# Kernel optimization log

Hardware: AMD Instinct MI355X
Metric: run time of the kernel (lower is better)

The kernel has to match this reference:

```python
import jax, jax.numpy as jnp
import numpy as np

N = 50000   # nodes
K = 8       # fixed in-degree per node (edges sorted by target)
NQ = 400000 # quadruplets
TWO_PI = 2.0 * np.pi


def setup_inputs() -> dict:
    key = jax.random.key(0)
    k1, k2 = jax.random.split(key)
    pos = jax.random.normal(k1, (N, 3), dtype=jnp.float32) * 3.0
    # ring-structured graph: node i receives edges from (i+1..i+K) mod N.
    # Edges sorted by target i with exactly K per node -> edges into node n
    # occupy slots [n*K, n*K+K). Since N > 2K, a node is never its own
    # 2-hop self (idx_i != idx_k always holds, matching torch's mask).
    i = np.repeat(np.arange(N, dtype=np.int32), K)
    d = np.tile(np.arange(1, K + 1, dtype=np.int32), N)
    j = (i + d) % N
    edge_index = jnp.asarray(np.stack([j, i]), dtype=jnp.int32)  # [2, E]
    q_index = jax.random.randint(k2, (4, NQ), 0, N, dtype=jnp.int32)
    return {"pos": pos, "edge_index": edge_index, "q_index": q_index}


def _geometry(pos, edge_index, q_index):
    j, i = edge_index[0], edge_index[1]
    E = j.shape[0]

    rel = pos[i] - pos[j]
    dist = jnp.sqrt(jnp.sum(rel * rel, axis=-1))                 # [E]

    # ---- triplets: for edge e=(j->i), k ranges over in-neighbors of j ----
    ar = jnp.arange(K, dtype=j.dtype)
    idx_kj = (j[:, None] * K + ar[None, :]).reshape(-1)          # [T] edge ids k->j
    idx_ji = jnp.repeat(jnp.arange(E, dtype=j.dtype), K)         # [T] edge ids j->i
    idx_i = i[idx_ji]
    idx_j = j[idx_ji]
    idx_k = j[idx_kj]

    pos_ji = pos[idx_i] - pos[idx_j]                             # [T,3]
    pos_jk = pos[idx_k] - pos[idx_j]                             # [T,3]
    a = jnp.sum(pos_ji * pos_jk, axis=-1)
    b = jnp.linalg.norm(jnp.cross(pos_ji, pos_jk), axis=-1)
    angle = jnp.arctan2(b, a)                                    # [T]

    # ---- quadruplets: k_n ranges over the K in-neighbors of idx_j ----
    kn_edges = idx_j[:, None] * K + ar[None, :]                  # [T,K]
    idx_k_n = j[kn_edges]                                        # [T,K]
    pos_jkn = pos[idx_k_n] - pos[idx_j][:, None, :]              # [T,K,3]
    plane1 = jnp.cross(pos_ji, pos_jk)                           # [T,3]
    plane2 = jnp.cross(pos_ji[:, None, :], pos_jkn)              # [T,K,3]
    dist_ji = jnp.sqrt(jnp.sum(pos_ji * pos_ji, axis=-1))        # [T]
    a2 = jnp.sum(plane1[:, None, :] * plane2, axis=-1)           # [T,K]
    b2 = jnp.sum(jnp.cross(plane1[:, None, :], plane2) * pos_ji[:, None, :], axis=-1) / dist_ji[:, None]
    torsion = jnp.arctan2(b2, a2)
    torsion = jnp.where(torsion <= 0, torsion + TWO_PI, torsion)
    valid = (idx_k_n != idx_i[:, None]) & (idx_k_n != idx_k[:, None])
    # scatter_min over quadruplets grouped by triplet == masked row-min
    torsiona = jnp.min(jnp.where(valid, torsion, jnp.inf), axis=-1)  # [T]

    plane_s = 0.5 * jnp.sin(angle) * dist[idx_kj] * dist[idx_ji]     # [T]

    # ---- tetrahedron volumes for quadruplets q_index [4,NQ] ----
    pq = pos[q_index.T]                                          # [NQ,4,3]
    v1 = pq[:, 1] - pq[:, 0]
    v2 = pq[:, 2] - pq[:, 0]
    v3 = pq[:, 3] - pq[:, 0]
    volume = jnp.abs(jnp.sum(jnp.cross(v1, v2) * v3, axis=-1)) / 6.0  # [NQ]

    return dist, angle, torsiona, plane_s, volume, idx_ji, idx_kj


def reference(pos, edge_index, q_index):
    dist, angle, torsiona, plane_s, volume, idx_ji, idx_kj = _geometry(pos, edge_index, q_index)
    # matches torch return: (dist, angle, torsiona, torsiona, torsiona, plane_s, volume, idx_ji, idx_kj)
    return (dist, angle, torsiona, torsiona, torsiona, plane_s, volume, idx_ji, idx_kj)
```

## Files before the change

kernel.cpp:

```cpp
#include <hip/hip_runtime.h>

#define KDEG 8
constexpr float TWO_PI_F = 6.28318530717958647692f;
constexpr float PI_F = 3.14159265358979323846f;
constexpr float PI_2_F = 1.57079632679489661923f;
constexpr float BIG_F = 1000.0f;

struct F3 { float x, y, z; };
__device__ __forceinline__ F3 f3sub(F3 a, F3 b) { return {a.x - b.x, a.y - b.y, a.z - b.z}; }
__device__ __forceinline__ float f3dot(F3 a, F3 b) { return a.x * b.x + a.y * b.y + a.z * b.z; }
__device__ __forceinline__ F3 f3cross(F3 a, F3 b) {
  return {a.y * b.z - a.z * b.y, a.z * b.x - a.x * b.z, a.x * b.y - a.y * b.x};
}
__device__ __forceinline__ F3 ldpos(const float* __restrict__ p, int idx) {
  return {p[3 * idx], p[3 * idx + 1], p[3 * idx + 2]};
}

__device__ __forceinline__ float fast_atan01(float z) {
  float z2 = z * z;
  return z * fmaf(z2, -0.19194795f, 0.97239411f);
}

__device__ __forceinline__ float fast_atan2(float y, float x) {
  float ax = fabsf(x), ay = fabsf(y);
  float mx = fmaxf(ax, ay);
  float mn = fminf(ax, ay);
  float z = mn * __builtin_amdgcn_rcpf(fmaxf(mx, 1e-30f));
  float r = fast_atan01(z);
  r = (ay > ax) ? (PI_2_F - r) : r;
  r = (x < 0.0f) ? (PI_F - r) : r;
  return (y < 0.0f) ? -r : r;
}

__device__ __forceinline__ float fast_atan2_pos(float y, float x) {
  float ax = fabsf(x);
  float mx = fmaxf(ax, y);
  float mn = fminf(ax, y);
  float z = mn * __builtin_amdgcn_rcpf(fmaxf(mx, 1e-30f));
  float r = fast_atan01(z);
  r = (y > ax) ? (PI_2_F - r) : r;
  return (x < 0.0f) ? (PI_F - r) : r;
}

__device__ __forceinline__ void st4(float* p, float a, float b, float c, float d) {
  float4 v = {a, b, c, d};
  *reinterpret_cast<float4*>(p) = v;
}

__device__ __forceinline__ void edge_work(
    int e,
    const float* __restrict__ pos,
    const int* __restrict__ ei_j,
    const int* __restrict__ ei_i,
    float* __restrict__ out,
    int off_angle, int off_t0, int off_t1, int off_t2,
    int off_ps, int off_iji, int off_ikj)
{
  int j = ei_j[e];
  int i = ei_i[e];
  (void)i;

  int base = j * KDEG;
  int nbr[KDEG];
#pragma unroll
  for (int n = 0; n < KDEG; n++) nbr[n] = ei_j[base + n];

  F3 pj = ldpos(pos, j);
  F3 pi = ldpos(pos, i);
  F3 pji = f3sub(pi, pj);
  float d2 = f3dot(pji, pji);
  float inv_dji = rsqrtf(d2);
  float dji = d2 * inv_dji;
  out[e] = dji;

  const F3 G = {0.53452248f, -0.26726124f, 0.80178373f};
  F3 e1 = f3cross(pji, G);
  F3 e2 = f3cross(pji, e1);
  float L2 = f3dot(e1, e1);
  float invL = rsqrtf(fmaxf(L2, 1e-30f));
  float djinvL = dji * invL;

  float phi[KDEG], phiw[KDEG], ang[KDEG], hb[KDEG];
#pragma unroll
  for (int n = 0; n < KDEG; n++) {
    F3 u = f3sub(ldpos(pos, nbr[n]), pj);
    float s = f3dot(pji, u);
    float a = f3dot(e1, u);
    float b = f3dot(e2, u) * inv_dji;
    phi[n] = fast_atan2(b, a);
    phiw[n] = phi[n] + TWO_PI_F;
    float perp = sqrtf(fmaf(a, a, b * b));
    float bfull = perp * djinvL;
    ang[n] = fast_atan2_pos(bfull, s);
    hb[n] = 0.5f * bfull;
  }

  int t0 = e * KDEG;
  st4(out + off_angle + t0,     ang[0], ang[1], ang[2], ang[3]);
  st4(out + off_angle + t0 + 4, ang[4], ang[5], ang[6], ang[7]);
  st4(out + off_ps + t0,        hb[0], hb[1], hb[2], hb[3]);
  st4(out + off_ps + t0 + 4,    hb[4], hb[5], hb[6], hb[7]);
  float fe = (float)e;
  st4(out + off_iji + t0,     fe, fe, fe, fe);
  st4(out + off_iji + t0 + 4, fe, fe, fe, fe);
  float fb = (float)base;
  st4(out + off_ikj + t0,     fb, fb + 1.0f, fb + 2.0f, fb + 3.0f);
  st4(out + off_ikj + t0 + 4, fb + 4.0f, fb + 5.0f, fb + 6.0f, fb + 7.0f);

  float succ[KDEG];
#pragma unroll
  for (int n = 0; n < KDEG; n++) succ[n] = BIG_F;
#pragma unroll
  for (int kk = 0; kk < KDEG; kk++) {
#pragma unroll
    for (int n = kk + 1; n < KDEG; n++) {
      bool gt = phi[n] > phi[kk];
      float ckk = gt ? phi[n] : phiw[n];
      float cn  = gt ? phiw[kk] : phi[kk];
      succ[kk] = fminf(succ[kk], ckk);
      succ[n]  = fminf(succ[n], cn);
    }
  }
  float mn[KDEG];
#pragma unroll
  for (int n = 0; n < KDEG; n++) mn[n] = succ[n] - phi[n];

  st4(out + off_t0 + t0,     mn[0], mn[1], mn[2], mn[3]);
  st4(out + off_t0 + t0 + 4, mn[4], mn[5], mn[6], mn[7]);
  st4(out + off_t1 + t0,     mn[0], mn[1], mn[2], mn[3]);
  st4(out + off_t1 + t0 + 4, mn[4], mn[5], mn[6], mn[7]);
  st4(out + off_t2 + t0,     mn[0], mn[1], mn[2], mn[3]);
  st4(out + off_t2 + t0 + 4, mn[4], mn[5], mn[6], mn[7]);
}

__device__ __forceinline__ void volume_work(
    int t,
    const float* __restrict__ pos,
    const int* __restrict__ q,
    float* __restrict__ out,
    int NQ, int off_vol)
{
  int q0 = q[t];
  int q1 = q[t + NQ];
  int q2 = q[t + 2 * NQ];
  int q3 = q[t + 3 * NQ];
  F3 p0 = ldpos(pos, q0);
  F3 p1 = ldpos(pos, q1);
  F3 p2 = ldpos(pos, q2);
  F3 p3 = ldpos(pos, q3);
  F3 v1 = f3sub(p1, p0);
  F3 v2 = f3sub(p2, p0);
  F3 v3 = f3sub(p3, p0);
  float vol = fabsf(f3dot(f3cross(v1, v2), v3)) * (1.0f / 6.0f);
  out[off_vol + t] = vol;
}

__global__ __launch_bounds__(256) void fused_kernel(
    const float* __restrict__ pos,
    const int* __restrict__ ei_j,
    const int* __restrict__ ei_i,
    const int* __restrict__ q,
    float* __restrict__ out,
    int E, int NQ, int nbE,
    int off_angle, int off_t0, int off_t1, int off_t2,
    int off_ps, int off_vol, int off_iji, int off_ikj)
{
  int b = blockIdx.x;
  if (b < nbE) {
    int e = b * blockDim.x + threadIdx.x;
    if (e < E)
      edge_work(e, pos, ei_j, ei_i, out,
                off_angle, off_t0, off_t1, off_t2, off_ps, off_iji, off_ikj);
  } else {
    int t = (b - nbE) * blockDim.x + threadIdx.x;
    if (t < NQ)
      volume_work(t, pos, q, out, NQ, off_vol);
  }
}

extern "C" void kernel_launch(void* const* d_in, const int* in_sizes, int n_in,
                              void* d_out, int out_size, void* d_ws, size_t ws_size,
                              hipStream_t stream) {
  const float* pos = (const float*)d_in[0];
  const int* edge_index = (const int*)d_in[1];
  const int* q_index = (const int*)d_in[2];

  const int E = in_sizes[1] / 2;
  const int NQ = in_sizes[2] / 4;
  const int T = E * KDEG;

  const int* ei_j = edge_index;
  const int* ei_i = edge_index + E;

  float* out = (float*)d_out;

  const int off_angle = E;
  const int off_t0 = off_angle + T;
  const int off_t1 = off_t0 + T;
  const int off_t2 = off_t1 + T;
  const int off_ps = off_t2 + T;
  const int off_vol = off_ps + T;
  const int off_iji = off_vol + NQ;
  const int off_ikj = off_iji + T;
  (void)out_size; (void)d_ws; (void)ws_size; (void)n_in;

  const int blk = 256;
  const int nbE = (E + blk - 1) / blk;
  const int nbQ = (NQ + blk - 1) / blk;

  fused_kernel<<<nbE + nbQ, blk, 0, stream>>>(
      pos, ei_j, ei_i, q_index, out, E, NQ, nbE,
      off_angle, off_t0, off_t1, off_t2, off_ps, off_vol, off_iji, off_ikj);
}
```

Measured before the change: 31.49 us.

## Map one thread per triplet and compute torsion min via lane shuffles

Replaces the one-thread-per-edge mapping, where each thread handled all 8 triplets, with one thread per triplet. The eight threads of an edge exchange their phi values through __shfl_xor to find the angular successor. This raises parallelism eightfold, lowers per-thread register pressure and gives coalesced scalar stores in place of per-thread float4 stores. In exchange, the edge-level loads and the basis setup are repeated in every triplet thread, and the total thread count grows.

```diff
diff --git a/kernel.cpp b/kernel.cpp
--- a/kernel.cpp
+++ b/kernel.cpp
@@ -42,13 +42,8 @@
   return (x < 0.0f) ? (PI_F - r) : r;
 }
 
-__device__ __forceinline__ void st4(float* p, float a, float b, float c, float d) {
-  float4 v = {a, b, c, d};
-  *reinterpret_cast<float4*>(p) = v;
-}
-
-__device__ __forceinline__ void edge_work(
-    int e,
+__device__ __forceinline__ void tri_work(
+    int t,
     const float* __restrict__ pos,
     const int* __restrict__ ei_j,
     const int* __restrict__ ei_i,
@@ -56,22 +51,18 @@
     int off_angle, int off_t0, int off_t1, int off_t2,
     int off_ps, int off_iji, int off_ikj)
 {
+  int e = t >> 3;
+  int kk = t & 7;
+
   int j = ei_j[e];
   int i = ei_i[e];
-  (void)i;
-
-  int base = j * KDEG;
-  int nbr[KDEG];
-#pragma unroll
-  for (int n = 0; n < KDEG; n++) nbr[n] = ei_j[base + n];
-
   F3 pj = ldpos(pos, j);
   F3 pi = ldpos(pos, i);
   F3 pji = f3sub(pi, pj);
   float d2 = f3dot(pji, pji);
   float inv_dji = rsqrtf(d2);
   float dji = d2 * inv_dji;
-  out[e] = dji;
+  if (kk == 0) out[e] = dji;
 
   const F3 G = {0.53452248f, -0.26726124f, 0.80178373f};
   F3 e1 = f3cross(pji, G);
@@ -80,57 +71,33 @@
   float invL = rsqrtf(fmaxf(L2, 1e-30f));
   float djinvL = dji * invL;
 
-  float phi[KDEG], phiw[KDEG], ang[KDEG], hb[KDEG];
+  int k = ei_j[j * KDEG + kk];
+  F3 u = f3sub(ldpos(pos, k), pj);
+  float s = f3dot(pji, u);
+  float a = f3dot(e1, u);
+  float b = f3dot(e2, u) * inv_dji;
+  float phi = fast_atan2(b, a);
+  float perp = sqrtf(fmaf(a, a, b * b));
+  float bfull = perp * djinvL;
+  float ang = fast_atan2_pos(bfull, s);
+  float hb = 0.5f * bfull;
+
+  float succ = BIG_F;
 #pragma unroll
-  for (int n = 0; n < KDEG; n++) {
-    F3 u = f3sub(ldpos(pos, nbr[n]), pj);
-    float s = f3dot(pji, u);
-    float a = f3dot(e1, u);
-    float b = f3dot(e2, u) * inv_dji;
-    phi[n] = fast_atan2(b, a);
-    phiw[n] = phi[n] + TWO_PI_F;
-    float perp = sqrtf(fmaf(a, a, b * b));
-    float bfull = perp * djinvL;
-    ang[n] = fast_atan2_pos(bfull, s);
-    hb[n] = 0.5f * bfull;
+  for (int m = 1; m < KDEG; m++) {
+    float php = __shfl_xor(phi, m, KDEG);
+    float cand = (php > phi) ? php : php + TWO_PI_F;
+    succ = fminf(succ, cand);
   }
+  float tors = succ - phi;
 
-  int t0 = e * KDEG;
-  st4(out + off_angle + t0,     ang[0], ang[1], ang[2], ang[3]);
-  st4(out + off_angle + t0 + 4, ang[4], ang[5], ang[6], ang[7]);
-  st4(out + off_ps + t0,        hb[0], hb[1], hb[2], hb[3]);
-  st4(out + off_ps + t0 + 4,    hb[4], hb[5], hb[6], hb[7]);
-  float fe = (float)e;
-  st4(out + off_iji + t0,     fe, fe, fe, fe);
-  st4(out + off_iji + t0 + 4, fe, fe, fe, fe);
-  float fb = (float)base;
-  st4(out + off_ikj + t0,     fb, fb + 1.0f, fb + 2.0f, fb + 3.0f);
-  st4(out + off_ikj + t0 + 4, fb + 4.0f, fb + 5.0f, fb + 6.0f, fb + 7.0f);
-
-  float succ[KDEG];
-#pragma unroll
-  for (int n = 0; n < KDEG; n++) succ[n] = BIG_F;
-#pragma unroll
-  for (int kk = 0; kk < KDEG; kk++) {
-#pragma unroll
-    for (int n = kk + 1; n < KDEG; n++) {
-      bool gt = phi[n] > phi[kk];
-      float ckk = gt ? phi[n] : phiw[n];
-      float cn  = gt ? phiw[kk] : phi[kk];
-      succ[kk] = fminf(succ[kk], ckk);
-      succ[n]  = fminf(succ[n], cn);
-    }
-  }
-  float mn[KDEG];
-#pragma unroll
-  for (int n = 0; n < KDEG; n++) mn[n] = succ[n] - phi[n];
-
-  st4(out + off_t0 + t0,     mn[0], mn[1], mn[2], mn[3]);
-  st4(out + off_t0 + t0 + 4, mn[4], mn[5], mn[6], mn[7]);
-  st4(out + off_t1 + t0,     mn[0], mn[1], mn[2], mn[3]);
-  st4(out + off_t1 + t0 + 4, mn[4], mn[5], mn[6], mn[7]);
-  st4(out + off_t2 + t0,     mn[0], mn[1], mn[2], mn[3]);
-  st4(out + off_t2 + t0 + 4, mn[4], mn[5], mn[6], mn[7]);
+  out[off_angle + t] = ang;
+  out[off_t0 + t] = tors;
+  out[off_t1 + t] = tors;
+  out[off_t2 + t] = tors;
+  out[off_ps + t] = hb;
+  out[off_iji + t] = (float)e;
+  out[off_ikj + t] = (float)(j * KDEG + kk);
 }
 
 __device__ __forceinline__ void volume_work(
@@ -161,18 +128,18 @@
     const int* __restrict__ ei_i,
     const int* __restrict__ q,
     float* __restrict__ out,
-    int E, int NQ, int nbE,
+    int T, int NQ, int nbT,
     int off_angle, int off_t0, int off_t1, int off_t2,
     int off_ps, int off_vol, int off_iji, int off_ikj)
 {
   int b = blockIdx.x;
-  if (b < nbE) {
-    int e = b * blockDim.x + threadIdx.x;
-    if (e < E)
-      edge_work(e, pos, ei_j, ei_i, out,
-                off_angle, off_t0, off_t1, off_t2, off_ps, off_iji, off_ikj);
+  if (b < nbT) {
+    int t = b * blockDim.x + threadIdx.x;
+    if (t < T)
+      tri_work(t, pos, ei_j, ei_i, out,
+               off_angle, off_t0, off_t1, off_t2, off_ps, off_iji, off_ikj);
   } else {
-    int t = (b - nbE) * blockDim.x + threadIdx.x;
+    int t = (b - nbT) * blockDim.x + threadIdx.x;
     if (t < NQ)
       volume_work(t, pos, q, out, NQ, off_vol);
   }
@@ -205,10 +172,10 @@
   (void)out_size; (void)d_ws; (void)ws_size; (void)n_in;
 
   const int blk = 256;
-  const int nbE = (E + blk - 1) / blk;
+  const int nbT = (T + blk - 1) / blk;
   const int nbQ = (NQ + blk - 1) / blk;
 
-  fused_kernel<<<nbE + nbQ, blk, 0, stream>>>(
-      pos, ei_j, ei_i, q_index, out, E, NQ, nbE,
+  fused_kernel<<<nbT + nbQ, blk, 0, stream>>>(
+      pos, ei_j, ei_i, q_index, out, T, NQ, nbT,
       off_angle, off_t0, off_t1, off_t2, off_ps, off_vol, off_iji, off_ikj);
 }
```

New measurement: 31.97 us. Within noise of the previous version (+1.5%).
